# Kernel optimization log

Hardware: AMD Instinct MI355X
Metric: run time of the kernel (lower is better)

The kernel has to match this reference:

```python
import jax, jax.numpy as jnp
import numpy as np

N_NODES = 50000
N_EDGES = 1600000
HID = 128
N_LAYERS = 3
N_GRAPHS = 64
LN_EPS = 1e-5


def setup_inputs() -> dict:
    key = jax.random.key(0)
    ks = jax.random.split(key, 8)
    x = jax.random.normal(ks[0], (N_NODES, HID), dtype=jnp.float32)
    edge_index = jax.random.randint(ks[1], (2, N_EDGES), 0, N_NODES)
    batch = jnp.sort(jax.random.randint(ks[2], (N_NODES,), 0, N_GRAPHS))
    s = 1.0 / np.sqrt(HID)
    Wn = jax.random.normal(ks[3], (N_LAYERS, HID, HID), dtype=jnp.float32) * s   # lin_l (neighbors)
    bn = jnp.zeros((N_LAYERS, HID), dtype=jnp.float32)                           # lin_l bias
    Wr = jax.random.normal(ks[4], (N_LAYERS, HID, HID), dtype=jnp.float32) * s   # lin_r (root), no bias
    gamma = jnp.ones((N_LAYERS, HID), dtype=jnp.float32)
    beta = jnp.zeros((N_LAYERS, HID), dtype=jnp.float32)
    return {"x": x, "Wn": Wn, "bn": bn, "Wr": Wr, "gamma": gamma, "beta": beta,
            "edge_index": edge_index, "batch": batch}


def _layer_norm(h, g, b):
    mu = jnp.mean(h, axis=-1, keepdims=True)
    var = jnp.mean((h - mu) ** 2, axis=-1, keepdims=True)
    return (h - mu) * jax.lax.rsqrt(var + LN_EPS) * g + b


def reference(x, Wn, bn, Wr, gamma, beta, edge_index, batch):
    src, dst = edge_index[0], edge_index[1]
    N = x.shape[0]
    # in-degree for mean aggregation (clamped to avoid div-by-zero for isolated nodes)
    deg = jax.ops.segment_sum(jnp.ones((src.shape[0],), x.dtype), dst, num_segments=N)
    inv_deg = 1.0 / jnp.maximum(deg, 1.0)
    for l in range(N_LAYERS):
        # SAGEConv: lin_l(mean_neighbor) + lin_r(x)
        agg = jax.ops.segment_sum(x[src], dst, num_segments=N) * inv_deg[:, None]
        h = agg @ Wn[l] + bn[l] + x @ Wr[l]
        h = _layer_norm(h, gamma[l], beta[l])
        x = jax.nn.relu(h)  # dropout is identity in eval mode
    node_emb = x
    cnt = jax.ops.segment_sum(jnp.ones((N,), x.dtype), batch, num_segments=N_GRAPHS)
    graph_emb = jax.ops.segment_sum(node_emb, batch, num_segments=N_GRAPHS) / jnp.maximum(cnt, 1.0)[:, None]
    return graph_emb, node_emb
```

## Files before the change

### kernel.cpp

```cpp
#include <hip/hip_runtime.h>

#define N_NODES 50000
#define N_EDGES 1600000
#define HID     128
#define N_GRAPHS 64

#define HB 200
#define EPB (N_EDGES / HB)
#define HWORDS 12500
#define NPP 12500
#define CWPP (NPP / 4)
#define NGRP 8
#define SPG (HB / NGRP)
#define NQ 4
#define QN (N_NODES / NQ)

#define WS_DEG   0u
#define WS_BSUM  50000u
#define WS_BOFF  50256u
#define WS_OFFS  50512u
#define WS_INVD  100512u
#define WS_CSR   150512u
#define WS_QOFF  950512u
#define WS_XB_B  1750512u
#define WS_GSUM  (WS_XB_B + 2500000u)
#define WS_XB_A  4950512u
#define WS_WP    8150512u
#define WS_END   8199664u

typedef __attribute__((ext_vector_type(8))) short short8;
typedef __attribute__((ext_vector_type(4))) float floatx4;

__device__ __forceinline__ float bf_lo(unsigned u) { return __uint_as_float(u << 16); }
__device__ __forceinline__ float bf_hi(unsigned u) { return __uint_as_float(u & 0xffff0000u); }
__device__ __forceinline__ unsigned bf_rn(float f) {
    unsigned u = __float_as_uint(f);
    unsigned r = ((u >> 16) & 1u) + 0x7fffu;
    return (u + r) >> 16;
}
__device__ __forceinline__ unsigned bf_pack(float lo, float hi) {
    return bf_rn(lo) | (bf_rn(hi) << 16);
}

__global__ __launch_bounds__(256) void k_prep(const float4* __restrict__ x, uint2* __restrict__ o,
                                              const float* __restrict__ Wn, const float* __restrict__ Wr,
                                              uint4* __restrict__ wp, const int* __restrict__ ei,
                                              unsigned* __restrict__ hist) {
    __shared__ unsigned sh[HWORDS];
    if (blockIdx.x < 6250) {
        int i = blockIdx.x * 256 + threadIdx.x;
        float4 v = x[i];
        uint2 r;
        r.x = bf_pack(v.x, v.y);
        r.y = bf_pack(v.z, v.w);
        o[i] = r;
    } else if (blockIdx.x < 6298) {
        int idx = (blockIdx.x - 6250) * 256 + threadIdx.x;
        int layer = idx >> 12;
        int rem = idx & 4095;
        int kb = rem >> 9;
        int n = (rem >> 2) & 127;
        int quad = rem & 3;
        float v[8];
#pragma unroll
        for (int j = 0; j < 8; j++) {
            int k = kb * 32 + quad * 8 + j;
            v[j] = (k < 128) ? Wn[layer * 16384 + k * 128 + n]
                             : Wr[layer * 16384 + (k - 128) * 128 + n];
        }
        uint4 r;
        r.x = bf_pack(v[0], v[1]);
        r.y = bf_pack(v[2], v[3]);
        r.z = bf_pack(v[4], v[5]);
        r.w = bf_pack(v[6], v[7]);
        wp[idx] = r;
    } else {
        const int hb = blockIdx.x - 6298;
        for (int i = threadIdx.x; i < HWORDS; i += 256) sh[i] = 0;
        __syncthreads();
        const int e0 = hb * EPB;
        for (int i = threadIdx.x; i < EPB; i += 256) {
            int d = __builtin_nontemporal_load(ei + N_EDGES + e0 + i);
            atomicAdd(&sh[d >> 2], 1u << ((d & 3) << 3));
        }
        __syncthreads();
        unsigned* hp = hist + (size_t)hb * HWORDS;
        for (int i = threadIdx.x; i < HWORDS; i += 256) hp[i] = sh[i];
    }
}


__global__ __launch_bounds__(256) void k_scanb1(unsigned* __restrict__ hist, unsigned* __restrict__ gsum) {
    int wb = blockIdx.x % 49;
    int g = blockIdx.x / 49;
    int w = wb * 256 + threadIdx.x;
    if (w >= HWORDS) return;
    size_t base = (size_t)(g * SPG) * HWORDS + w;
    unsigned run = 0;
#pragma unroll 5
    for (int b = 0; b < SPG; ++b) {
        unsigned u = hist[base + (size_t)b * HWORDS];
        hist[base + (size_t)b * HWORDS] = run;
        run += u;
    }
    gsum[(size_t)g * HWORDS + w] = run;
}

__global__ __launch_bounds__(256) void k_scanb2(unsigned* __restrict__ gsum, int* __restrict__ deg,
                                                int* __restrict__ bsum) {
    int w = blockIdx.x * 256 + threadIdx.x;
    int mysum = 0;
    if (w < HWORDS) {
        unsigned run = 0;
#pragma unroll
        for (int g = 0; g < NGRP; ++g) {
            unsigned u = gsum[(size_t)g * HWORDS + w];
            gsum[(size_t)g * HWORDS + w] = run;
            run += u;
        }
#pragma unroll
        for (int k = 0; k < 4; ++k) {
            int d = (int)((run >> (k << 3)) & 0xffu);
            deg[4 * w + k] = d;
            mysum += d;
        }
    }
    __shared__ int s[256];
    s[threadIdx.x] = mysum;
    __syncthreads();
    for (int d = 128; d > 0; d >>= 1) {
        if (threadIdx.x < d) s[threadIdx.x] += s[threadIdx.x + d];
        __syncthreads();
    }
    if (threadIdx.x == 0) bsum[blockIdx.x] = s[0];
}

__global__ __launch_bounds__(256) void k_offsets(const int* __restrict__ deg, const int* __restrict__ bsum,
                                                 int* __restrict__ offs, float* __restrict__ invdeg) {
    __shared__ int sb[64], sb0[64];
    __shared__ int s[256];
    int b = blockIdx.x, t = threadIdx.x;
    if (t < 64) {
        int v = (t < 49) ? bsum[t] : 0;
        sb[t] = v;
        sb0[t] = v;
    }
    __syncthreads();
    for (int d = 1; d < 64; d <<= 1) {
        int add = (t < 64 && t >= d) ? sb[t - d] : 0;
        __syncthreads();
        if (t < 64) sb[t] += add;
        __syncthreads();
    }
    int n0 = (b * 256 + t) * 4;
    int dl[4] = {0, 0, 0, 0};
#pragma unroll
    for (int k = 0; k < 4; ++k)
        if (n0 + k < N_NODES) dl[k] = deg[n0 + k];
    int v = dl[0] + dl[1] + dl[2] + dl[3];
    s[t] = v;
    __syncthreads();
    for (int dd = 1; dd < 256; dd <<= 1) {
        int add = (t >= dd) ? s[t - dd] : 0;
        __syncthreads();
        s[t] += add;
        __syncthreads();
    }
    int base = (sb[b] - sb0[b]) + s[t] - v;
#pragma unroll
    for (int k = 0; k < 4; ++k) {
        if (n0 + k < N_NODES) {
            offs[n0 + k] = base;
            invdeg[n0 + k] = 1.0f / fmaxf((float)dl[k], 1.0f);
            base += dl[k];
        }
    }
}

__global__ __launch_bounds__(256) void k_fill(const int* __restrict__ ei, const int* __restrict__ offs,
                                              const unsigned* __restrict__ hist,
                                              const unsigned* __restrict__ gpre,
                                              unsigned short* __restrict__ csr) {
    __shared__ unsigned scur[CWPP];
    const int pass = blockIdx.x & 3;
    const int b = blockIdx.x >> 2;
    const int nbase = pass * NPP;
    const unsigned* hb = hist + (size_t)b * HWORDS + pass * CWPP;
    const unsigned* gb = gpre + (size_t)(b / SPG) * HWORDS + pass * CWPP;
    for (int i = threadIdx.x; i < CWPP; i += 256) scur[i] = hb[i] + gb[i];
    __syncthreads();
    const int e0 = b * EPB;
    for (int i = threadIdx.x; i < EPB; i += 256) {
        int d = __builtin_nontemporal_load(ei + N_EDGES + e0 + i);
        unsigned rd = (unsigned)(d - nbase);
        if (rd < (unsigned)NPP) {
            int s = ei[e0 + i];
            int sh = (rd & 3) << 3;
            unsigned old = atomicAdd(&scur[rd >> 2], 1u << sh);
            unsigned rel = (old >> sh) & 0xffu;
            csr[offs[d] + (int)rel] = (unsigned short)s;
        }
    }
}

__global__ __launch_bounds__(256) void k_qsort(unsigned short* __restrict__ csr,
                                               const int* __restrict__ offs,
                                               const int* __restrict__ deg,
                                               unsigned* __restrict__ qoff) {
    __shared__ unsigned short seg[16][256];
    __shared__ int cnt[16][4];
    __shared__ int st[16][4];
    const int t = threadIdx.x;
    const int g = t >> 4;
    const int l = t & 15;
    const int node = blockIdx.x * 16 + g;
    const int beg = offs[node];
    const int dn = deg[node];
    if (l < 4) cnt[g][l] = 0;
    __syncthreads();
    for (int j = l; j < dn; j += 16) {
        unsigned short s = csr[beg + j];
        seg[g][j] = s;
        atomicAdd(&cnt[g][s / QN], 1);
    }
    __syncthreads();
    if (l == 0) {
        int c0 = cnt[g][0], c1 = cnt[g][1], c2 = cnt[g][2];
        st[g][0] = 0;
        st[g][1] = c0;
        st[g][2] = c0 + c1;
        st[g][3] = c0 + c1 + c2;
    }
    __syncthreads();
    if (t < 4) {
#pragma unroll
        for (int p = 0; p < 3; ++p) {
            unsigned wv = 0;
#pragma unroll
            for (int k = 0; k < 4; ++k)
                wv |= ((unsigned)st[t * 4 + k][p + 1] & 0xffu) << (k << 3);
            qoff[(size_t)p * HWORDS + blockIdx.x * 4 + t] = wv;
        }
    }
    if (l < 4) cnt[g][l] = st[g][l];
    __syncthreads();
    for (int j = l; j < dn; j += 16) {
        unsigned short s = seg[g][j];
        int pos = atomicAdd(&cnt[g][s / QN], 1);
        csr[beg + pos] = s;
    }
}

__global__ __launch_bounds__(256) void k_layer16(
        const uint4* __restrict__ xq, const unsigned short* __restrict__ csr,
        const int* __restrict__ offs, const int* __restrict__ deg,
        const unsigned* __restrict__ qoff, const float* __restrict__ invdeg,
        const uint4* __restrict__ wp, const float* __restrict__ bn,
        const float* __restrict__ gam, const float* __restrict__ bet,
        float* __restrict__ xout, unsigned* __restrict__ b16out, int write_f32) {
    __shared__ float H[16 * 132];
    uint4* A = (uint4*)H;

    const int t = threadIdx.x;
    const int wv = t >> 6;
    const int lane = t & 63;
    const int slot = lane >> 4;
    const int m = lane & 15;
    const int n0 = blockIdx.x * 16;
    const uint4* xm = xq + m;

    const int node = n0 + wv * 4 + slot;
    const int beg = offs[node];
    const int dtot = deg[node];
    const int wrd = node >> 2;
    const int sh8 = (node & 3) << 3;
    const int q1 = (qoff[0 * HWORDS + wrd] >> sh8) & 0xff;
    const int q2 = (qoff[1 * HWORDS + wrd] >> sh8) & 0xff;
    const int q3 = (qoff[2 * HWORDS + wrd] >> sh8) & 0xff;

    float a0 = 0.f, a1 = 0.f, a2 = 0.f, a3 = 0.f, a4 = 0.f, a5 = 0.f, a6 = 0.f, a7 = 0.f;

#define SEG_GATHER(JB, JE)                                                        \
    {                                                                             \
        int j = (JB);                                                             \
        const int e = (JE);                                                       \
        for (; j + 8 <= e; j += 8) {                                              \
            int s0 = csr[j] << 4;                                                 \
            int s1 = csr[j + 1] << 4;                                             \
            int s2 = csr[j + 2] << 4;                                             \
            int s3 = csr[j + 3] << 4;                                             \
            int s4 = csr[j + 4] << 4;                                             \
            int s5 = csr[j + 5] << 4;                                             \
            int s6 = csr[j + 6] << 4;                                             \
            int s7 = csr[j + 7] << 4;                                             \
            uint4 u0 = xm[s0], u1 = xm[s1], u2 = xm[s2], u3 = xm[s3];             \
            uint4 u4 = xm[s4], u5 = xm[s5], u6 = xm[s6], u7 = xm[s7];             \
            a0 += ((bf_lo(u0.x) + bf_lo(u1.x)) + (bf_lo(u2.x) + bf_lo(u3.x)))     \
                + ((bf_lo(u4.x) + bf_lo(u5.x)) + (bf_lo(u6.x) + bf_lo(u7.x)));    \
            a1 += ((bf_hi(u0.x) + bf_hi(u1.x)) + (bf_hi(u2.x) + bf_hi(u3.x)))     \
                + ((bf_hi(u4.x) + bf_hi(u5.x)) + (bf_hi(u6.x) + bf_hi(u7.x)));    \
            a2 += ((bf_lo(u0.y) + bf_lo(u1.y)) + (bf_lo(u2.y) + bf_lo(u3.y)))     \
                + ((bf_lo(u4.y) + bf_lo(u5.y)) + (bf_lo(u6.y) + bf_lo(u7.y)));    \
            a3 += ((bf_hi(u0.y) + bf_hi(u1.y)) + (bf_hi(u2.y) + bf_hi(u3.y)))     \
                + ((bf_hi(u4.y) + bf_hi(u5.y)) + (bf_hi(u6.y) + bf_hi(u7.y)));    \
            a4 += ((bf_lo(u0.z) + bf_lo(u1.z)) + (bf_lo(u2.z) + bf_lo(u3.z)))     \
                + ((bf_lo(u4.z) + bf_lo(u5.z)) + (bf_lo(u6.z) + bf_lo(u7.z)));    \
            a5 += ((bf_hi(u0.z) + bf_hi(u1.z)) + (bf_hi(u2.z) + bf_hi(u3.z)))     \
                + ((bf_hi(u4.z) + bf_hi(u5.z)) + (bf_hi(u6.z) + bf_hi(u7.z)));    \
            a6 += ((bf_lo(u0.w) + bf_lo(u1.w)) + (bf_lo(u2.w) + bf_lo(u3.w)))     \
                + ((bf_lo(u4.w) + bf_lo(u5.w)) + (bf_lo(u6.w) + bf_lo(u7.w)));    \
            a7 += ((bf_hi(u0.w) + bf_hi(u1.w)) + (bf_hi(u2.w) + bf_hi(u3.w)))     \
                + ((bf_hi(u4.w) + bf_hi(u5.w)) + (bf_hi(u6.w) + bf_hi(u7.w)));    \
        }                                                                         \
        for (; j + 4 <= e; j += 4) {                                              \
            int s0 = csr[j] << 4;                                                 \
            int s1 = csr[j + 1] << 4;                                             \
            int s2 = csr[j + 2] << 4;                                             \
            int s3 = csr[j + 3] << 4;                                             \
            uint4 u0 = xm[s0], u1 = xm[s1], u2 = xm[s2], u3 = xm[s3];             \
            a0 += (bf_lo(u0.x) + bf_lo(u1.x)) + (bf_lo(u2.x) + bf_lo(u3.x));      \
            a1 += (bf_hi(u0.x) + bf_hi(u1.x)) + (bf_hi(u2.x) + bf_hi(u3.x));      \
            a2 += (bf_lo(u0.y) + bf_lo(u1.y)) + (bf_lo(u2.y) + bf_lo(u3.y));      \
            a3 += (bf_hi(u0.y) + bf_hi(u1.y)) + (bf_hi(u2.y) + bf_hi(u3.y));      \
            a4 += (bf_lo(u0.z) + bf_lo(u1.z)) + (bf_lo(u2.z) + bf_lo(u3.z));      \
            a5 += (bf_hi(u0.z) + bf_hi(u1.z)) + (bf_hi(u2.z) + bf_hi(u3.z));      \
            a6 += (bf_lo(u0.w) + bf_lo(u1.w)) + (bf_lo(u2.w) + bf_lo(u3.w));      \
            a7 += (bf_hi(u0.w) + bf_hi(u1.w)) + (bf_hi(u2.w) + bf_hi(u3.w));      \
        }                                                                         \
        for (; j < e; ++j) {                                                      \
            uint4 u0 = xm[csr[j] << 4];                                           \
            a0 += bf_lo(u0.x); a1 += bf_hi(u0.x);                                 \
            a2 += bf_lo(u0.y); a3 += bf_hi(u0.y);                                 \
            a4 += bf_lo(u0.z); a5 += bf_hi(u0.z);                                 \
            a6 += bf_lo(u0.w); a7 += bf_hi(u0.w);                                 \
        }                                                                         \
    }

    SEG_GATHER(beg, beg + q1)
    __syncthreads();
    SEG_GATHER(beg + q1, beg + q2)
    __syncthreads();
    SEG_GATHER(beg + q2, beg + q3)
    __syncthreads();
    SEG_GATHER(beg + q3, beg + dtot)

    {
        float id = invdeg[node];
        uint4 r;
        r.x = bf_pack(a0 * id, a1 * id);
        r.y = bf_pack(a2 * id, a3 * id);
        r.z = bf_pack(a4 * id, a5 * id);
        r.w = bf_pack(a6 * id, a7 * id);
        A[(wv * 4 + slot) * 17 + m] = r;
    }
    __syncthreads();

    const int quad = lane >> 4;
    const int nl = lane & 15;
    const int nb = wv * 32;
    floatx4 acc0 = {0.f, 0.f, 0.f, 0.f}, acc1 = acc0;
#pragma unroll
    for (int kb = 0; kb < 8; ++kb) {
        uint4 av = (kb < 4) ? A[nl * 17 + kb * 4 + quad]
                            : xq[(n0 + nl) * 16 + (kb - 4) * 4 + quad];
        uint4 b0 = wp[(kb * 128 + nb + nl) * 4 + quad];
        uint4 b1 = wp[(kb * 128 + nb + 16 + nl) * 4 + quad];
        short8 as = *(short8*)&av;
        short8 b0s = *(short8*)&b0, b1s = *(short8*)&b1;
        acc0 = __builtin_amdgcn_mfma_f32_16x16x32_bf16(as, b0s, acc0, 0, 0, 0);
        acc1 = __builtin_amdgcn_mfma_f32_16x16x32_bf16(as, b1s, acc1, 0, 0, 0);
    }
    __syncthreads();

    float bn0 = bn[nb + nl];
    float bn1 = bn[nb + 16 + nl];
#pragma unroll
    for (int reg = 0; reg < 4; ++reg) {
        int rr = quad * 4 + reg;
        H[rr * 132 + nb + nl] = acc0[reg] + bn0;
        H[rr * 132 + nb + 16 + nl] = acc1[reg] + bn1;
    }
    __syncthreads();

    const int row = t >> 4;
    const int sub = t & 15;
    const float* hr = &H[row * 132 + sub * 8];
    float v[8];
    float s = 0.f, s2 = 0.f;
#pragma unroll
    for (int i = 0; i < 8; i++) {
        v[i] = hr[i];
        s += v[i];
        s2 += v[i] * v[i];
    }
#pragma unroll
    for (int msk = 1; msk < 16; msk <<= 1) {
        s += __shfl_xor(s, msk);
        s2 += __shfl_xor(s2, msk);
    }
    float mean = s * (1.f / 128.f);
    float var = s2 * (1.f / 128.f) - mean * mean;
    float rstd = rsqrtf(var + 1e-5f);
    const int gr = n0 + row;
    const int cb = sub * 8;
    float o[8];
#pragma unroll
    for (int i = 0; i < 8; i++)
        o[i] = fmaxf((v[i] - mean) * rstd * gam[cb + i] + bet[cb + i], 0.f);
    if (write_f32) {
        *(float4*)&xout[(size_t)gr * HID + cb] = *(float4*)&o[0];
        *(float4*)&xout[(size_t)gr * HID + cb + 4] = *(float4*)&o[4];
    }
    unsigned p[4];
#pragma unroll
    for (int i = 0; i < 4; i++) p[i] = bf_pack(o[2 * i], o[2 * i + 1]);
    *(uint4*)&b16out[(size_t)gr * 64 + (cb >> 1)] = *(uint4*)&p[0];
}


__global__ __launch_bounds__(1024) void k_pool1(const unsigned* __restrict__ xb,
                                                const int* __restrict__ batch,
                                                float* __restrict__ partial, int* __restrict__ cnt) {
    const int bid = blockIdx.x;
    const int g = bid >> 2;
    const int part = bid & 3;
    __shared__ int s_beg, s_end;
    if (threadIdx.x == 0) {
        int lo = 0, hi = N_NODES;
        while (lo < hi) { int mid = (lo + hi) >> 1; if (batch[mid] < g) lo = mid + 1; else hi = mid; }
        s_beg = lo;
        lo = 0; hi = N_NODES;
        while (lo < hi) { int mid = (lo + hi) >> 1; if (batch[mid] < g + 1) lo = mid + 1; else hi = mid; }
        s_end = lo;
    }
    __syncthreads();
    const int beg = s_beg, end = s_end;
    const int w = threadIdx.x & 63;
    const int q = threadIdx.x >> 6;
    float ax = 0.f, ay = 0.f;
    for (int r = beg + part * 16 + q; r < end; r += 64) {
        unsigned u = __builtin_nontemporal_load(xb + (size_t)r * 64 + w);
        ax += bf_lo(u);
        ay += bf_hi(u);
    }
    __shared__ float sx[16][64], sy[16][64];
    sx[q][w] = ax;
    sy[q][w] = ay;
    __syncthreads();
    if (q == 0) {
        float tx = 0.f, ty = 0.f;
#pragma unroll
        for (int i = 0; i < 16; i++) { tx += sx[i][w]; ty += sy[i][w]; }
        float2 r;
        r.x = tx;
        r.y = ty;
        *(float2*)&partial[(size_t)bid * 128 + w * 2] = r;
    }
    if (part == 0 && threadIdx.x == 0) cnt[g] = end - beg;
}

__global__ __launch_bounds__(256) void k_pool2(const float* __restrict__ partial,
                                               const int* __restrict__ cnt,
                                               float* __restrict__ out) {
    int idx = blockIdx.x * 256 + threadIdx.x;
    int g = idx >> 7;
    float s = partial[(size_t)(g * 4 + 0) * 128 + (idx & 127)]
            + partial[(size_t)(g * 4 + 1) * 128 + (idx & 127)]
            + partial[(size_t)(g * 4 + 2) * 128 + (idx & 127)]
            + partial[(size_t)(g * 4 + 3) * 128 + (idx & 127)];
    out[idx] = s / fmaxf((float)cnt[g], 1.f);
}

extern "C" void kernel_launch(void* const* d_in, const int* in_sizes, int n_in,
                              void* d_out, int out_size, void* d_ws, size_t ws_size,
                              hipStream_t stream) {
    const float* x0 = (const float*)d_in[0];
    const float* Wn = (const float*)d_in[1];
    const float* bn = (const float*)d_in[2];
    const float* Wr = (const float*)d_in[3];
    const float* gam = (const float*)d_in[4];
    const float* bet = (const float*)d_in[5];
    const int* ei = (const int*)d_in[6];
    const int* batch = (const int*)d_in[7];

    float* out = (float*)d_out;
    float* node_out = out + N_GRAPHS * HID;

    unsigned* ws = (unsigned*)d_ws;
    int* deg = (int*)(ws + WS_DEG);
    int* bsum = (int*)(ws + WS_BSUM);
    int* offs = (int*)(ws + WS_OFFS);
    float* invdeg = (float*)(ws + WS_INVD);
    unsigned short* csr = (unsigned short*)(ws + WS_CSR);
    unsigned* qoff = ws + WS_QOFF;
    unsigned* hist = ws + WS_XB_B;
    unsigned* gsum = ws + WS_GSUM;
    unsigned* xa = ws + WS_XB_A;
    unsigned* xbb = ws + WS_XB_B;
    uint4* wp = (uint4*)(ws + WS_WP);
    float* partial = (float*)(ws + WS_CSR);
    int* cnt = (int*)(ws + WS_CSR + 256 * 128);

    k_prep<<<6498, 256, 0, stream>>>((const float4*)x0, (uint2*)xa, Wn, Wr, wp, ei, hist);
    k_scanb1<<<NGRP * 49, 256, 0, stream>>>(hist, gsum);
    k_scanb2<<<49, 256, 0, stream>>>(gsum, deg, bsum);
    k_offsets<<<49, 256, 0, stream>>>(deg, bsum, offs, invdeg);
    k_fill<<<HB * 4, 256, 0, stream>>>(ei, offs, hist, gsum, csr);
    k_qsort<<<N_NODES / 16, 256, 0, stream>>>(csr, offs, deg, qoff);

    const int lb = N_NODES / 16;

    for (int l = 0; l < 3; ++l) {
        const unsigned* xin = (l & 1) ? xbb : xa;
        unsigned* xout16 = (l & 1) ? xa : xbb;
        k_layer16<<<lb, 256, 0, stream>>>((const uint4*)xin, csr, offs, deg, qoff, invdeg,
                                          wp + (size_t)l * 4096, bn + (size_t)l * HID,
                                          gam + (size_t)l * HID, bet + (size_t)l * HID,
                                          node_out, xout16, l == 2 ? 1 : 0);
    }

    k_pool1<<<N_GRAPHS * 4, 1024, 0, stream>>>(xbb, batch, partial, cnt);
    k_pool2<<<32, 256, 0, stream>>>(partial, cnt, out);
}
```

Baseline: 446.5 us.

## Fuse per-node quadrant sort of CSR into the first layer kernel

Result: faster. 432.6 us (-3.1%).

```diff
diff --git a/kernel.cpp b/kernel.cpp
--- a/kernel.cpp
+++ b/kernel.cpp
@@ -203,62 +203,17 @@
     }
 }
 
-__global__ __launch_bounds__(256) void k_qsort(unsigned short* __restrict__ csr,
-                                               const int* __restrict__ offs,
-                                               const int* __restrict__ deg,
-                                               unsigned* __restrict__ qoff) {
-    __shared__ unsigned short seg[16][256];
-    __shared__ int cnt[16][4];
-    __shared__ int st[16][4];
-    const int t = threadIdx.x;
-    const int g = t >> 4;
-    const int l = t & 15;
-    const int node = blockIdx.x * 16 + g;
-    const int beg = offs[node];
-    const int dn = deg[node];
-    if (l < 4) cnt[g][l] = 0;
-    __syncthreads();
-    for (int j = l; j < dn; j += 16) {
-        unsigned short s = csr[beg + j];
-        seg[g][j] = s;
-        atomicAdd(&cnt[g][s / QN], 1);
-    }
-    __syncthreads();
-    if (l == 0) {
-        int c0 = cnt[g][0], c1 = cnt[g][1], c2 = cnt[g][2];
-        st[g][0] = 0;
-        st[g][1] = c0;
-        st[g][2] = c0 + c1;
-        st[g][3] = c0 + c1 + c2;
-    }
-    __syncthreads();
-    if (t < 4) {
-#pragma unroll
-        for (int p = 0; p < 3; ++p) {
-            unsigned wv = 0;
-#pragma unroll
-            for (int k = 0; k < 4; ++k)
-                wv |= ((unsigned)st[t * 4 + k][p + 1] & 0xffu) << (k << 3);
-            qoff[(size_t)p * HWORDS + blockIdx.x * 4 + t] = wv;
-        }
-    }
-    if (l < 4) cnt[g][l] = st[g][l];
-    __syncthreads();
-    for (int j = l; j < dn; j += 16) {
-        unsigned short s = seg[g][j];
-        int pos = atomicAdd(&cnt[g][s / QN], 1);
-        csr[beg + pos] = s;
-    }
-}
-
 __global__ __launch_bounds__(256) void k_layer16(
-        const uint4* __restrict__ xq, const unsigned short* __restrict__ csr,
+        const uint4* __restrict__ xq, unsigned short* __restrict__ csr,
         const int* __restrict__ offs, const int* __restrict__ deg,
-        const unsigned* __restrict__ qoff, const float* __restrict__ invdeg,
+        unsigned* __restrict__ qoff, const float* __restrict__ invdeg,
         const uint4* __restrict__ wp, const float* __restrict__ bn,
         const float* __restrict__ gam, const float* __restrict__ bet,
-        float* __restrict__ xout, unsigned* __restrict__ b16out, int write_f32) {
+        float* __restrict__ xout, unsigned* __restrict__ b16out,
+        int write_f32, int sort_first) {
     __shared__ float H[16 * 132];
+    __shared__ unsigned short seg[16][256];
+    __shared__ int cnt[16][4], st[16][4];
     uint4* A = (uint4*)H;
 
     const int t = threadIdx.x;
@@ -269,80 +224,151 @@
     const int n0 = blockIdx.x * 16;
     const uint4* xm = xq + m;
 
-    const int node = n0 + wv * 4 + slot;
+    const int gi = wv * 4 + slot;
+    const int node = n0 + gi;
     const int beg = offs[node];
     const int dtot = deg[node];
-    const int wrd = node >> 2;
-    const int sh8 = (node & 3) << 3;
-    const int q1 = (qoff[0 * HWORDS + wrd] >> sh8) & 0xff;
-    const int q2 = (qoff[1 * HWORDS + wrd] >> sh8) & 0xff;
-    const int q3 = (qoff[2 * HWORDS + wrd] >> sh8) & 0xff;
 
     float a0 = 0.f, a1 = 0.f, a2 = 0.f, a3 = 0.f, a4 = 0.f, a5 = 0.f, a6 = 0.f, a7 = 0.f;
 
-#define SEG_GATHER(JB, JE)                                                        \
+#define GBODY8(u0, u1, u2, u3, u4, u5, u6, u7)                                    \
+    a0 += ((bf_lo(u0.x) + bf_lo(u1.x)) + (bf_lo(u2.x) + bf_lo(u3.x)))             \
+        + ((bf_lo(u4.x) + bf_lo(u5.x)) + (bf_lo(u6.x) + bf_lo(u7.x)));            \
+    a1 += ((bf_hi(u0.x) + bf_hi(u1.x)) + (bf_hi(u2.x) + bf_hi(u3.x)))             \
+        + ((bf_hi(u4.x) + bf_hi(u5.x)) + (bf_hi(u6.x) + bf_hi(u7.x)));            \
+    a2 += ((bf_lo(u0.y) + bf_lo(u1.y)) + (bf_lo(u2.y) + bf_lo(u3.y)))             \
+        + ((bf_lo(u4.y) + bf_lo(u5.y)) + (bf_lo(u6.y) + bf_lo(u7.y)));            \
+    a3 += ((bf_hi(u0.y) + bf_hi(u1.y)) + (bf_hi(u2.y) + bf_hi(u3.y)))             \
+        + ((bf_hi(u4.y) + bf_hi(u5.y)) + (bf_hi(u6.y) + bf_hi(u7.y)));            \
+    a4 += ((bf_lo(u0.z) + bf_lo(u1.z)) + (bf_lo(u2.z) + bf_lo(u3.z)))             \
+        + ((bf_lo(u4.z) + bf_lo(u5.z)) + (bf_lo(u6.z) + bf_lo(u7.z)));            \
+    a5 += ((bf_hi(u0.z) + bf_hi(u1.z)) + (bf_hi(u2.z) + bf_hi(u3.z)))             \
+        + ((bf_hi(u4.z) + bf_hi(u5.z)) + (bf_hi(u6.z) + bf_hi(u7.z)));            \
+    a6 += ((bf_lo(u0.w) + bf_lo(u1.w)) + (bf_lo(u2.w) + bf_lo(u3.w)))             \
+        + ((bf_lo(u4.w) + bf_lo(u5.w)) + (bf_lo(u6.w) + bf_lo(u7.w)));            \
+    a7 += ((bf_hi(u0.w) + bf_hi(u1.w)) + (bf_hi(u2.w) + bf_hi(u3.w)))             \
+        + ((bf_hi(u4.w) + bf_hi(u5.w)) + (bf_hi(u6.w) + bf_hi(u7.w)));
+
+#define GBODY4(u0, u1, u2, u3)                                                    \
+    a0 += (bf_lo(u0.x) + bf_lo(u1.x)) + (bf_lo(u2.x) + bf_lo(u3.x));              \
+    a1 += (bf_hi(u0.x) + bf_hi(u1.x)) + (bf_hi(u2.x) + bf_hi(u3.x));              \
+    a2 += (bf_lo(u0.y) + bf_lo(u1.y)) + (bf_lo(u2.y) + bf_lo(u3.y));              \
+    a3 += (bf_hi(u0.y) + bf_hi(u1.y)) + (bf_hi(u2.y) + bf_hi(u3.y));              \
+    a4 += (bf_lo(u0.z) + bf_lo(u1.z)) + (bf_lo(u2.z) + bf_lo(u3.z));              \
+    a5 += (bf_hi(u0.z) + bf_hi(u1.z)) + (bf_hi(u2.z) + bf_hi(u3.z));              \
+    a6 += (bf_lo(u0.w) + bf_lo(u1.w)) + (bf_lo(u2.w) + bf_lo(u3.w));              \
+    a7 += (bf_hi(u0.w) + bf_hi(u1.w)) + (bf_hi(u2.w) + bf_hi(u3.w));
+
+#define GBODY1(u0)                                                                \
+    a0 += bf_lo(u0.x); a1 += bf_hi(u0.x);                                         \
+    a2 += bf_lo(u0.y); a3 += bf_hi(u0.y);                                         \
+    a4 += bf_lo(u0.z); a5 += bf_hi(u0.z);                                         \
+    a6 += bf_lo(u0.w); a7 += bf_hi(u0.w);
+
+#define SEG_GATHER(IDX, JB, JE)                                                   \
     {                                                                             \
         int j = (JB);                                                             \
         const int e = (JE);                                                       \
         for (; j + 8 <= e; j += 8) {                                              \
-            int s0 = csr[j] << 4;                                                 \
-            int s1 = csr[j + 1] << 4;                                             \
-            int s2 = csr[j + 2] << 4;                                             \
-            int s3 = csr[j + 3] << 4;                                             \
-            int s4 = csr[j + 4] << 4;                                             \
-            int s5 = csr[j + 5] << 4;                                             \
-            int s6 = csr[j + 6] << 4;                                             \
-            int s7 = csr[j + 7] << 4;                                             \
+            int s0 = IDX(j) << 4;                                                 \
+            int s1 = IDX(j + 1) << 4;                                             \
+            int s2 = IDX(j + 2) << 4;                                             \
+            int s3 = IDX(j + 3) << 4;                                             \
+            int s4 = IDX(j + 4) << 4;                                             \
+            int s5 = IDX(j + 5) << 4;                                             \
+            int s6 = IDX(j + 6) << 4;                                             \
+            int s7 = IDX(j + 7) << 4;                                             \
             uint4 u0 = xm[s0], u1 = xm[s1], u2 = xm[s2], u3 = xm[s3];             \
             uint4 u4 = xm[s4], u5 = xm[s5], u6 = xm[s6], u7 = xm[s7];             \
-            a0 += ((bf_lo(u0.x) + bf_lo(u1.x)) + (bf_lo(u2.x) + bf_lo(u3.x)))     \
-                + ((bf_lo(u4.x) + bf_lo(u5.x)) + (bf_lo(u6.x) + bf_lo(u7.x)));    \
-            a1 += ((bf_hi(u0.x) + bf_hi(u1.x)) + (bf_hi(u2.x) + bf_hi(u3.x)))     \
-                + ((bf_hi(u4.x) + bf_hi(u5.x)) + (bf_hi(u6.x) + bf_hi(u7.x)));    \
-            a2 += ((bf_lo(u0.y) + bf_lo(u1.y)) + (bf_lo(u2.y) + bf_lo(u3.y)))     \
-                + ((bf_lo(u4.y) + bf_lo(u5.y)) + (bf_lo(u6.y) + bf_lo(u7.y)));    \
-            a3 += ((bf_hi(u0.y) + bf_hi(u1.y)) + (bf_hi(u2.y) + bf_hi(u3.y)))     \
-                + ((bf_hi(u4.y) + bf_hi(u5.y)) + (bf_hi(u6.y) + bf_hi(u7.y)));    \
-            a4 += ((bf_lo(u0.z) + bf_lo(u1.z)) + (bf_lo(u2.z) + bf_lo(u3.z)))     \
-                + ((bf_lo(u4.z) + bf_lo(u5.z)) + (bf_lo(u6.z) + bf_lo(u7.z)));    \
-            a5 += ((bf_hi(u0.z) + bf_hi(u1.z)) + (bf_hi(u2.z) + bf_hi(u3.z)))     \
-                + ((bf_hi(u4.z) + bf_hi(u5.z)) + (bf_hi(u6.z) + bf_hi(u7.z)));    \
-            a6 += ((bf_lo(u0.w) + bf_lo(u1.w)) + (bf_lo(u2.w) + bf_lo(u3.w)))     \
-                + ((bf_lo(u4.w) + bf_lo(u5.w)) + (bf_lo(u6.w) + bf_lo(u7.w)));    \
-            a7 += ((bf_hi(u0.w) + bf_hi(u1.w)) + (bf_hi(u2.w) + bf_hi(u3.w)))     \
-                + ((bf_hi(u4.w) + bf_hi(u5.w)) + (bf_hi(u6.w) + bf_hi(u7.w)));    \
+            GBODY8(u0, u1, u2, u3, u4, u5, u6, u7)                                \
         }                                                                         \
         for (; j + 4 <= e; j += 4) {                                              \
-            int s0 = csr[j] << 4;                                                 \
-            int s1 = csr[j + 1] << 4;                                             \
-            int s2 = csr[j + 2] << 4;                                             \
-            int s3 = csr[j + 3] << 4;                                             \
+            int s0 = IDX(j) << 4;                                                 \
+            int s1 = IDX(j + 1) << 4;                                             \
+            int s2 = IDX(j + 2) << 4;                                             \
+            int s3 = IDX(j + 3) << 4;                                             \
             uint4 u0 = xm[s0], u1 = xm[s1], u2 = xm[s2], u3 = xm[s3];             \
-            a0 += (bf_lo(u0.x) + bf_lo(u1.x)) + (bf_lo(u2.x) + bf_lo(u3.x));      \
-            a1 += (bf_hi(u0.x) + bf_hi(u1.x)) + (bf_hi(u2.x) + bf_hi(u3.x));      \
-            a2 += (bf_lo(u0.y) + bf_lo(u1.y)) + (bf_lo(u2.y) + bf_lo(u3.y));      \
-            a3 += (bf_hi(u0.y) + bf_hi(u1.y)) + (bf_hi(u2.y) + bf_hi(u3.y));      \
-            a4 += (bf_lo(u0.z) + bf_lo(u1.z)) + (bf_lo(u2.z) + bf_lo(u3.z));      \
-            a5 += (bf_hi(u0.z) + bf_hi(u1.z)) + (bf_hi(u2.z) + bf_hi(u3.z));      \
-            a6 += (bf_lo(u0.w) + bf_lo(u1.w)) + (bf_lo(u2.w) + bf_lo(u3.w));      \
-            a7 += (bf_hi(u0.w) + bf_hi(u1.w)) + (bf_hi(u2.w) + bf_hi(u3.w));      \
+            GBODY4(u0, u1, u2, u3)                                                \
         }                                                                         \
         for (; j < e; ++j) {                                                      \
-            uint4 u0 = xm[csr[j] << 4];                                           \
-            a0 += bf_lo(u0.x); a1 += bf_hi(u0.x);                                 \
-            a2 += bf_lo(u0.y); a3 += bf_hi(u0.y);                                 \
-            a4 += bf_lo(u0.z); a5 += bf_hi(u0.z);                                 \
-            a6 += bf_lo(u0.w); a7 += bf_hi(u0.w);                                 \
+            uint4 u0 = xm[IDX(j) << 4];                                           \
+            GBODY1(u0)                                                            \
         }                                                                         \
     }
 
-    SEG_GATHER(beg, beg + q1)
-    __syncthreads();
-    SEG_GATHER(beg + q1, beg + q2)
-    __syncthreads();
-    SEG_GATHER(beg + q2, beg + q3)
-    __syncthreads();
-    SEG_GATHER(beg + q3, beg + dtot)
+#define IDX_G(j) ((int)csr[beg + (j)])
+#define IDX_L(j) ((int)seg[gi][(j)])
+
+    int q1, q2, q3;
+    if (sort_first) {
+        if (m < 4) cnt[gi][m] = 0;
+        for (int j = m; j < dtot; j += 16) {
+            unsigned short v = csr[beg + j];
+            seg[gi][j] = v;
+            atomicAdd(&cnt[gi][(int)v / QN], 1);
+        }
+        if (m == 0) {
+            int c0 = cnt[gi][0], c1 = cnt[gi][1], c2 = cnt[gi][2];
+            st[gi][0] = 0; st[gi][1] = c0; st[gi][2] = c0 + c1; st[gi][3] = c0 + c1 + c2;
+            cnt[gi][0] = 0; cnt[gi][1] = c0; cnt[gi][2] = c0 + c1; cnt[gi][3] = c0 + c1 + c2;
+        }
+        unsigned val2[8];
+#pragma unroll
+        for (int i = 0; i < 8; ++i) {
+            int j0 = m + 32 * i, j1 = j0 + 16;
+            unsigned v0 = (j0 < dtot) ? (unsigned)seg[gi][j0] : 0u;
+            unsigned v1 = (j1 < dtot) ? (unsigned)seg[gi][j1] : 0u;
+            val2[i] = v0 | (v1 << 16);
+        }
+#pragma unroll
+        for (int i = 0; i < 8; ++i) {
+            int j0 = m + 32 * i, j1 = j0 + 16;
+            if (j0 < dtot) {
+                unsigned v0 = val2[i] & 0xffffu;
+                int pos = atomicAdd(&cnt[gi][(int)v0 / QN], 1);
+                seg[gi][pos] = (unsigned short)v0;
+            }
+            if (j1 < dtot) {
+                unsigned v1 = val2[i] >> 16;
+                int pos = atomicAdd(&cnt[gi][(int)v1 / QN], 1);
+                seg[gi][pos] = (unsigned short)v1;
+            }
+        }
+        for (int j = m; j < dtot; j += 16)
+            csr[beg + j] = seg[gi][j];
+        q1 = st[gi][1]; q2 = st[gi][2]; q3 = st[gi][3];
+        __syncthreads();
+        if (t < 4) {
+#pragma unroll
+            for (int p = 0; p < 3; ++p) {
+                unsigned wvq = 0;
+#pragma unroll
+                for (int k = 0; k < 4; ++k)
+                    wvq |= ((unsigned)st[t * 4 + k][p + 1] & 0xffu) << (k << 3);
+                qoff[(size_t)p * HWORDS + blockIdx.x * 4 + t] = wvq;
+            }
+        }
+        SEG_GATHER(IDX_L, 0, q1)
+        __syncthreads();
+        SEG_GATHER(IDX_L, q1, q2)
+        __syncthreads();
+        SEG_GATHER(IDX_L, q2, q3)
+        __syncthreads();
+        SEG_GATHER(IDX_L, q3, dtot)
+    } else {
+        const int wrd = node >> 2;
+        const int sh8 = (node & 3) << 3;
+        q1 = (qoff[0 * HWORDS + wrd] >> sh8) & 0xff;
+        q2 = (qoff[1 * HWORDS + wrd] >> sh8) & 0xff;
+        q3 = (qoff[2 * HWORDS + wrd] >> sh8) & 0xff;
+        SEG_GATHER(IDX_G, 0, q1)
+        __syncthreads();
+        SEG_GATHER(IDX_G, q1, q2)
+        __syncthreads();
+        SEG_GATHER(IDX_G, q2, q3)
+        __syncthreads();
+        SEG_GATHER(IDX_G, q3, dtot)
+    }
 
     {
         float id = invdeg[node];
@@ -351,7 +377,7 @@
         r.y = bf_pack(a2 * id, a3 * id);
         r.z = bf_pack(a4 * id, a5 * id);
         r.w = bf_pack(a6 * id, a7 * id);
-        A[(wv * 4 + slot) * 17 + m] = r;
+        A[gi * 17 + m] = r;
     }
     __syncthreads();
 
@@ -506,7 +532,6 @@
     k_scanb2<<<49, 256, 0, stream>>>(gsum, deg, bsum);
     k_offsets<<<49, 256, 0, stream>>>(deg, bsum, offs, invdeg);
     k_fill<<<HB * 4, 256, 0, stream>>>(ei, offs, hist, gsum, csr);
-    k_qsort<<<N_NODES / 16, 256, 0, stream>>>(csr, offs, deg, qoff);
 
     const int lb = N_NODES / 16;
 
@@ -516,7 +541,7 @@
         k_layer16<<<lb, 256, 0, stream>>>((const uint4*)xin, csr, offs, deg, qoff, invdeg,
                                           wp + (size_t)l * 4096, bn + (size_t)l * HID,
                                           gam + (size_t)l * HID, bet + (size_t)l * HID,
-                                          node_out, xout16, l == 2 ? 1 : 0);
+                                          node_out, xout16, l == 2 ? 1 : 0, l == 0 ? 1 : 0);
     }
 
     k_pool1<<<N_GRAPHS * 4, 1024, 0, stream>>>(xbb, batch, partial, cnt);
```
